# Performance work log

Hardware: AMD Instinct MI355X
Metric: run time of the kernel (lower is better)

Reference implementation:

```python
import jax, jax.numpy as jnp
import numpy as np

EPS = 1e-6
B, N, E = 2, 100000, 400000
NODE_DIM, NUM_FEAT = 32, 32
H0, H1 = 128, 64   # state_encoder_hidden_size
D = 64             # gcn_node_dim


def setup_inputs() -> dict:
    key = jax.random.key(0)
    ks = jax.random.split(key, 12)
    def lin(k, fan_in, shape):
        b = 1.0 / np.sqrt(fan_in)
        return jax.random.uniform(k, shape, jnp.float32, -b, b)
    return {
        "numerical": jax.random.normal(ks[0], (B, NUM_FEAT), jnp.float32),
        "node_feature": jax.random.normal(ks[1], (B, N, NODE_DIM), jnp.float32),
        "edge_index": jax.random.randint(ks[2], (B, E, 2), 0, N),
        "edge_mask": jax.random.randint(ks[3], (B, E), 0, 2).astype(bool),
        "stage": jax.random.normal(ks[4], (B, 2), jnp.float32),
        # numerical feature encoder: Linear(32->128) tanh, Linear(128->64) tanh
        "W1": lin(ks[5], NUM_FEAT, (NUM_FEAT, H0)), "b1": lin(ks[6], NUM_FEAT, (H0,)),
        "W2": lin(ks[7], H0, (H0, H1)), "b2": lin(ks[8], H0, (H1,)),
        # node encoder: Linear(32->64) tanh
        "Wn": lin(ks[9], NODE_DIM, (NODE_DIM, D)), "bn": lin(ks[10], NODE_DIM, (D,)),
        # edge_fc: Linear(128->64) tanh
        "We": lin(ks[11], 2 * D, (2 * D, D)),
        "be": lin(jax.random.fold_in(key, 99), 2 * D, (D,)),
    }


def reference(numerical, node_feature, edge_index, edge_mask, stage,
              W1, b1, W2, b2, Wn, bn, We, be):
    # numerical feature encoder
    h_num = jnp.tanh(jnp.tanh(numerical @ W1 + b1) @ W2 + b2)       # [B, H1]
    # node encoder
    h_nodes = jnp.tanh(node_feature @ Wn + bn)                       # [B, N, D]
    # gather node feats to edge endpoints
    h1 = jnp.take_along_axis(h_nodes, edge_index[:, :, 0:1], axis=1)  # [B, E, D]
    h2 = jnp.take_along_axis(h_nodes, edge_index[:, :, 1:2], axis=1)  # [B, E, D]
    # edge_fc applied to [h1,h2] and [h2,h1], averaged. Split We to avoid concat.
    Wa, Wb = We[:D], We[D:]
    e12 = jnp.tanh(h1 @ Wa + h2 @ Wb + be)
    e21 = jnp.tanh(h2 @ Wa + h1 @ Wb + be)
    h_edges = 0.5 * (e12 + e21)                                       # [B, E, D]
    m = edge_mask[:, :, None]
    h_edges = jnp.where(m, h_edges, 0.0)
    # masked mean over edges
    mf = edge_mask.astype(h_edges.dtype)
    h_mean = (h_edges * mf[:, :, None]).sum(axis=1) / mf.sum(axis=1, keepdims=True)
    state_value = jnp.concatenate([h_num, h_mean, stage], axis=-1)    # [B, H1+D+2]
    state_policy = h_edges                                            # [B, E, D]
    return (state_policy, state_value)
```

## Files before the change

### kernel.cpp

```cpp
#include <hip/hip_runtime.h>
#include <hip/hip_bf16.h>

typedef __attribute__((ext_vector_type(4))) float  f32x4;
typedef __attribute__((ext_vector_type(8))) __bf16 bf16x8;

#define NB 2
#define NN 100000
#define NE 400000
#define EPB 256

__device__ __forceinline__ float tanh_f(float x) {
  float y = __builtin_amdgcn_fmed3f(2.f * x, -40.f, 40.f);
  float e = __expf(y);
  return fmaf(-2.f, __builtin_amdgcn_rcpf(e + 1.f), 1.f);
}

__device__ __forceinline__ float ldf(const void* p, long i, int bf) {
  return bf ? (float)((const __bf16*)p)[i] : ((const float*)p)[i];
}

__global__ __launch_bounds__(256) void k_setup(
    const unsigned int* __restrict__ mw, const unsigned int* __restrict__ nodew,
    const void* __restrict__ numerical, const void* __restrict__ W1,
    const void* __restrict__ b1, const void* __restrict__ W2,
    const void* __restrict__ b2, const void* __restrict__ Wn,
    const void* __restrict__ bn, const void* __restrict__ We,
    int* __restrict__ flags, float* __restrict__ hnum,
    float* __restrict__ sums, float* __restrict__ counts,
    __bf16* __restrict__ packWn, __bf16* __restrict__ packWe,
    float* __restrict__ packBn) {
  __shared__ int badS, goodS, dtS;
  __shared__ float numf[2][32];
  __shared__ float u[2][128];
  const int t = threadIdx.x;
  if (t == 0) { badS = 0; goodS = 0; }
  __syncthreads();
  int my = 0;
  for (int i = t; i < 4096; i += 256) my |= (mw[i] > 1u) ? 1 : 0;
  if (my) atomicOr(&badS, 1);
  int g = 0;
  for (int i = t; i < 4096; i += 256) {
    unsigned lo = nodew[i] & 0xFFFFu;
    unsigned e = (lo >> 7) & 0xFFu;
    g += (lo == 0u || (e >= 100u && e <= 141u)) ? 1 : 0;
  }
  atomicAdd(&goodS, g);
  __syncthreads();
  if (t == 0) {
    flags[0] = badS;
    dtS = (goodS > 2048) ? 1 : 0;
    flags[1] = dtS;
  }
  __syncthreads();
  const int dt = dtS;

  if (t < 128) sums[t] = 0.f;
  if (t < 2) counts[t] = 0.f;
  if (t < 64) numf[t >> 5][t & 31] = ldf(numerical, t, dt);
  __syncthreads();
  {
    const int b = t >> 7, j = t & 127;
    float acc = ldf(b1, j, dt);
#pragma unroll
    for (int k = 0; k < 32; ++k) acc += numf[b][k] * ldf(W1, k * 128 + j, dt);
    u[b][j] = tanh_f(acc);
  }
  __syncthreads();
  if (t < 128) {
    const int b = t >> 6, d = t & 63;
    float acc = ldf(b2, d, dt);
#pragma unroll
    for (int k = 0; k < 128; ++k) acc += u[b][k] * ldf(W2, k * 64 + d, dt);
    hnum[b * 64 + d] = tanh_f(acc);
  }

  if (t < 64) {
    const int m = t & 15, quad = t >> 4;
#pragma unroll
    for (int nt = 0; nt < 4; ++nt) {
      const int c = m + 16 * nt;
#pragma unroll
      for (int j = 0; j < 8; ++j)
        packWn[t * 32 + nt * 8 + j] = (__bf16)ldf(Wn, (quad * 8 + j) * 64 + c, dt);
      packBn[t * 4 + nt] = ldf(bn, c, dt);
    }
#pragma unroll
    for (int f = 0; f < 16; ++f) {
      const int s = f >> 2, nt = f & 3;
      const int n = m + 16 * nt;
#pragma unroll
      for (int j = 0; j < 8; ++j) {
        const int k = s * 32 + quad * 8 + j;
        packWe[(f * 64 + t) * 8 + j] = (__bf16)ldf(We, (long)k * 64 + n, dt);
      }
    }
  }
}

__global__ __launch_bounds__(256) void k_nodes(
    const void* __restrict__ node, const __bf16* __restrict__ packWn,
    const float* __restrict__ packBn, const int* __restrict__ flags,
    __bf16* __restrict__ hG) {
  const int t = threadIdx.x;
  const int wave = t >> 6, lane = t & 63;
  const int m = lane & 15, quad = lane >> 4;
  const int dt = flags[1];

  bf16x8 wnF[4];
#pragma unroll
  for (int nt = 0; nt < 4; ++nt)
    wnF[nt] = *(const bf16x8*)(packWn + lane * 32 + nt * 8);
  float bnv[4];
#pragma unroll
  for (int nt = 0; nt < 4; ++nt) bnv[nt] = packBn[lane * 4 + nt];

  const long r0 = ((long)blockIdx.x * 4 + wave) * 16;
  bf16x8 aF;
  if (dt) {
    aF = *(const bf16x8*)((const __bf16*)node + (r0 + m) * 32 + quad * 8);
  } else {
    const float* p = (const float*)node + (r0 + m) * 32 + quad * 8;
    f32x4 v0 = *(const f32x4*)p, v1 = *(const f32x4*)(p + 4);
#pragma unroll
    for (int j = 0; j < 4; ++j) { aF[j] = (__bf16)v0[j]; aF[4 + j] = (__bf16)v1[j]; }
  }

  f32x4 acc[4];
#pragma unroll
  for (int nt = 0; nt < 4; ++nt) {
    f32x4 c; c[0] = bnv[nt]; c[1] = bnv[nt]; c[2] = bnv[nt]; c[3] = bnv[nt];
    acc[nt] = c;
  }
#pragma unroll
  for (int nt = 0; nt < 4; ++nt)
    acc[nt] = __builtin_amdgcn_mfma_f32_16x16x32_bf16(aF, wnF[nt], acc[nt], 0, 0, 0);

  __bf16* out = hG + r0 * 64;
#pragma unroll
  for (int nt = 0; nt < 4; ++nt)
#pragma unroll
    for (int r = 0; r < 4; ++r)
      out[(quad * 4 + r) * 64 + m + 16 * nt] = (__bf16)tanh_f(acc[nt][r]);
}

__global__ __launch_bounds__(256) void k_edges(
    const int2* __restrict__ eidx, const void* __restrict__ emask,
    const int* __restrict__ flags, const __bf16* __restrict__ hG,
    const __bf16* __restrict__ packWe, const void* __restrict__ be,
    float* __restrict__ sums, float* __restrict__ counts,
    float* __restrict__ outp) {
  const int nbPerB = (NE + EPB - 1) / EPB;
  const int b = blockIdx.x / nbPerB;
  const long e0 = (long)(blockIdx.x % nbPerB) * EPB;
  const int t = threadIdx.x;
  const int wave = t >> 6, lane = t & 63;
  const int m = lane & 15, quad = lane >> 4;
  const int dt = flags[1], mode = flags[0];

  __shared__ __bf16 weL[64 * 128];
  __shared__ int2 eL[EPB];
  __shared__ float mL[EPB];
  __shared__ float red[4][64];
  __shared__ float redc[4];

  {
    const bf16x8* src = (const bf16x8*)packWe;
    bf16x8* dst = (bf16x8*)weL;
#pragma unroll
    for (int u = 0; u < 4; ++u) dst[t + 256 * u] = src[t + 256 * u];
  }
  {
    const long e = e0 + t;
    const int valid = (e < NE) ? 1 : 0;
    const long ec = valid ? e : (NE - 1);
    eL[t] = eidx[(long)b * NE + ec];
    float mv;
    if (mode) mv = (float)(((const unsigned char*)emask)[(long)b * NE + ec]);
    else      mv = (float)(((const int*)emask)[(long)b * NE + ec]);
    mL[t] = valid ? mv : 0.f;
  }
  __syncthreads();

  float be2[4];
#pragma unroll
  for (int nt = 0; nt < 4; ++nt) be2[nt] = 2.f * ldf(be, m + 16 * nt, dt);

  const __bf16* hb = hG + (long)b * NN * 64;
  float psum[4] = {0.f, 0.f, 0.f, 0.f};

  bf16x8 a0, a1, a2, a3;
  {
    const int2 ij = eL[wave * 64 + m];
    const __bf16* hi = hb + (long)ij.x * 64;
    const __bf16* hj = hb + (long)ij.y * 64;
    a0 = *(const bf16x8*)(hi + quad * 8);
    a1 = *(const bf16x8*)(hi + 32 + quad * 8);
    a2 = *(const bf16x8*)(hj + quad * 8);
    a3 = *(const bf16x8*)(hj + 32 + quad * 8);
  }

#pragma unroll
  for (int it = 0; it < 4; ++it) {
    const int slot = wave * 64 + it * 16;
    const bf16x8 c0 = a0, c1 = a1, c2 = a2, c3 = a3;
    if (it < 3) {
      const int2 ij = eL[slot + 16 + m];
      const __bf16* hi = hb + (long)ij.x * 64;
      const __bf16* hj = hb + (long)ij.y * 64;
      a0 = *(const bf16x8*)(hi + quad * 8);
      a1 = *(const bf16x8*)(hi + 32 + quad * 8);
      a2 = *(const bf16x8*)(hj + quad * 8);
      a3 = *(const bf16x8*)(hj + 32 + quad * 8);
    }

    f32x4 acc12[4], acc21[4];
#pragma unroll
    for (int nt = 0; nt < 4; ++nt) {
      f32x4 z; z[0] = 0.f; z[1] = 0.f; z[2] = 0.f; z[3] = 0.f;
      acc12[nt] = z; acc21[nt] = z;
    }
#pragma unroll
    for (int s = 0; s < 4; ++s) {
      bf16x8 w[4];
#pragma unroll
      for (int nt = 0; nt < 4; ++nt)
        w[nt] = *(const bf16x8*)(weL + ((4 * s + nt) * 64 + lane) * 8);
      const bf16x8 a12 = (s == 0) ? c0 : (s == 1) ? c1 : (s == 2) ? c2 : c3;
      const bf16x8 a21 = (s == 0) ? c2 : (s == 1) ? c3 : (s == 2) ? c0 : c1;
#pragma unroll
      for (int nt = 0; nt < 4; ++nt) {
        acc12[nt] = __builtin_amdgcn_mfma_f32_16x16x32_bf16(a12, w[nt], acc12[nt], 0, 0, 0);
        acc21[nt] = __builtin_amdgcn_mfma_f32_16x16x32_bf16(a21, w[nt], acc21[nt], 0, 0, 0);
      }
    }

    const long egbase = e0 + slot;
#pragma unroll
    for (int r = 0; r < 4; ++r) {
      const long e = egbase + quad * 4 + r;
      if (e >= NE) continue;
      const float mvr = mL[slot + quad * 4 + r];
      float* op = outp + ((long)b * NE + e) * 64 + m;
#pragma unroll
      for (int nt = 0; nt < 4; ++nt) {
        float x12 = __builtin_amdgcn_fmed3f(
            fmaf(acc12[nt][r], 2.f, be2[nt]), -40.f, 40.f);
        float x21 = __builtin_amdgcn_fmed3f(
            fmaf(acc21[nt][r], 2.f, be2[nt]), -40.f, 40.f);
        const float p12 = __builtin_amdgcn_rcpf(__expf(x12) + 1.f);
        const float p21 = __builtin_amdgcn_rcpf(__expf(x21) + 1.f);
        const float v = mvr * (1.f - p12 - p21);
        psum[nt] += v;
        __builtin_nontemporal_store(v, op + 16 * nt);
      }
    }
  }

#pragma unroll
  for (int nt = 0; nt < 4; ++nt) {
    psum[nt] += __shfl_xor(psum[nt], 16);
    psum[nt] += __shfl_xor(psum[nt], 32);
  }
  if (quad == 0) {
#pragma unroll
    for (int nt = 0; nt < 4; ++nt) red[wave][m + 16 * nt] = psum[nt];
  }
  float pc = mL[t];
#pragma unroll
  for (int d = 1; d < 64; d <<= 1) pc += __shfl_xor(pc, d);
  if (lane == 0) redc[wave] = pc;
  __syncthreads();
  if (t < 64) {
    const float s = red[0][t] + red[1][t] + red[2][t] + red[3][t];
    atomicAdd(&sums[b * 64 + t], s);
  }
  if (t == 0) atomicAdd(&counts[b], redc[0] + redc[1] + redc[2] + redc[3]);
}

__global__ __launch_bounds__(512) void k_final(
    const float* __restrict__ hnum, const float* __restrict__ sums,
    const float* __restrict__ counts, const void* __restrict__ stage,
    const int* __restrict__ flags, float* __restrict__ out) {
  const int t = threadIdx.x;
  const int dt = flags[1];
  if (t < 260) {
    const int b = t / 130, c = t % 130;
    float v;
    if (c < 64) v = hnum[b * 64 + c];
    else if (c < 128) v = sums[b * 64 + (c - 64)] / counts[b];
    else v = ldf(stage, b * 2 + (c - 128), dt);
    out[(long)NB * NE * 64 + (long)b * 130 + c] = v;
  }
}

extern "C" void kernel_launch(void* const* d_in, const int* in_sizes, int n_in,
                              void* d_out, int out_size, void* d_ws, size_t ws_size,
                              hipStream_t stream) {
  const void* numerical = d_in[0];
  const void* node      = d_in[1];
  const int2* eidx      = (const int2*)d_in[2];
  const void* emask     = d_in[3];
  const void* stage     = d_in[4];
  const void* W1 = d_in[5];
  const void* b1 = d_in[6];
  const void* W2 = d_in[7];
  const void* b2 = d_in[8];
  const void* Wn = d_in[9];
  const void* bn = d_in[10];
  const void* We = d_in[11];
  const void* be = d_in[12];

  char* ws = (char*)d_ws;
  int*    flags  = (int*)ws;
  float*  sums   = (float*)(ws + 256);
  float*  counts = (float*)(ws + 1024);
  float*  hnum   = (float*)(ws + 1280);
  float*  packBn = (float*)(ws + 2048);
  __bf16* packWn = (__bf16*)(ws + 4096);
  __bf16* packWe = (__bf16*)(ws + 8192);
  __bf16* hG     = (__bf16*)(ws + 32768);
  float*  outp   = (float*)d_out;

  k_setup<<<1, 256, 0, stream>>>((const unsigned int*)emask, (const unsigned int*)node,
                                 numerical, W1, b1, W2, b2, Wn, bn, We,
                                 flags, hnum, sums, counts, packWn, packWe, packBn);
  k_nodes<<<(NB * NN) / 64, 256, 0, stream>>>(node, packWn, packBn, flags, hG);
  k_edges<<<NB * ((NE + EPB - 1) / EPB), 256, 0, stream>>>(eidx, emask, flags, hG, packWe, be,
                                                           sums, counts, outp);
  k_final<<<1, 512, 0, stream>>>(hnum, sums, counts, stage, flags, outp);
}
```

Baseline: 392.4 us.

## Compact masked-in edges per block and skip gather/MFMA for masked edges

Each block now uses a wave ballot and prefix count to build a compacted list of edges whose mask is set. It writes zeros directly for masked-out edges and runs the node gather, MFMA and tanh only on the kept edges, spread across waves in 16-edge tiles. This removes the gather bandwidth and compute spent on the roughly half of edges that are masked out, at the cost of an extra barrier, shared-memory index indirection and less regular store addresses. The two tanh calls are merged algebraically so one reciprocal replaces two, and the weight-packing setup is spread over all 256 threads.

```diff
diff --git a/kernel.cpp b/kernel.cpp
--- a/kernel.cpp
+++ b/kernel.cpp
@@ -84,14 +84,18 @@
         packWn[t * 32 + nt * 8 + j] = (__bf16)ldf(Wn, (quad * 8 + j) * 64 + c, dt);
       packBn[t * 4 + nt] = ldf(bn, c, dt);
     }
-#pragma unroll
-    for (int f = 0; f < 16; ++f) {
-      const int s = f >> 2, nt = f & 3;
-      const int n = m + 16 * nt;
+  }
+  {
+    const int lane = t & 63, fg = t >> 6;
+    const int m2 = lane & 15, quad2 = lane >> 4;
+#pragma unroll
+    for (int ff = 0; ff < 4; ++ff) {
+      const int f = fg * 4 + ff;
+      const int n = m2 + 16 * ff;
 #pragma unroll
       for (int j = 0; j < 8; ++j) {
-        const int k = s * 32 + quad * 8 + j;
-        packWe[(f * 64 + t) * 8 + j] = (__bf16)ldf(We, (long)k * 64 + n, dt);
+        const int k = fg * 32 + quad2 * 8 + j;
+        packWe[(f * 64 + lane) * 8 + j] = (__bf16)ldf(We, (long)k * 64 + n, dt);
       }
     }
   }
@@ -160,8 +164,9 @@
   __shared__ __bf16 weL[64 * 128];
   __shared__ int2 eL[EPB];
   __shared__ float mL[EPB];
+  __shared__ unsigned short cS[EPB];
+  __shared__ int wcnt[4];
   __shared__ float red[4][64];
-  __shared__ float redc[4];
 
   {
     const bf16x8* src = (const bf16x8*)packWe;
@@ -169,6 +174,7 @@
 #pragma unroll
     for (int u = 0; u < 4; ++u) dst[t + 256 * u] = src[t + 256 * u];
   }
+  int kept;
   {
     const long e = e0 + t;
     const int valid = (e < NE) ? 1 : 0;
@@ -177,41 +183,69 @@
     float mv;
     if (mode) mv = (float)(((const unsigned char*)emask)[(long)b * NE + ec]);
     else      mv = (float)(((const int*)emask)[(long)b * NE + ec]);
-    mL[t] = valid ? mv : 0.f;
-  }
-  __syncthreads();
+    mv = valid ? mv : 0.f;
+    mL[t] = mv;
+    kept = (mv != 0.f) ? 1 : 0;
+  }
+  const unsigned long long bal = __ballot(kept);
+  const int lpos = __popcll(bal & ((1ull << lane) - 1ull));
+  if (lane == 0) wcnt[wave] = __popcll(bal);
+  __syncthreads();
+
+  int woff = 0, cntTot = 0;
+#pragma unroll
+  for (int w = 0; w < 4; ++w) {
+    cntTot += wcnt[w];
+    if (w < wave) woff += wcnt[w];
+  }
+  if (kept) cS[woff + lpos] = (unsigned short)t;
+
+  {
+    const int g = lane >> 2, gi = lane & 3;
+    const f32x4 z = {0.f, 0.f, 0.f, 0.f};
+#pragma unroll
+    for (int p = 0; p < 4; ++p) {
+      const int slot = wave * 64 + p * 16 + g;
+      const long e = e0 + slot;
+      if (e < NE && mL[slot] == 0.f) {
+        float* op = outp + ((long)b * NE + e) * 64 + gi * 16;
+        __builtin_nontemporal_store(z, (f32x4*)op);
+        __builtin_nontemporal_store(z, (f32x4*)(op + 4));
+        __builtin_nontemporal_store(z, (f32x4*)(op + 8));
+        __builtin_nontemporal_store(z, (f32x4*)(op + 12));
+      }
+    }
+  }
 
   float be2[4];
 #pragma unroll
   for (int nt = 0; nt < 4; ++nt) be2[nt] = 2.f * ldf(be, m + 16 * nt, dt);
+  __syncthreads();
 
   const __bf16* hb = hG + (long)b * NN * 64;
+  const int ntiles = (cntTot + 15) >> 4;
   float psum[4] = {0.f, 0.f, 0.f, 0.f};
 
   bf16x8 a0, a1, a2, a3;
-  {
-    const int2 ij = eL[wave * 64 + m];
-    const __bf16* hi = hb + (long)ij.x * 64;
-    const __bf16* hj = hb + (long)ij.y * 64;
-    a0 = *(const bf16x8*)(hi + quad * 8);
-    a1 = *(const bf16x8*)(hi + 32 + quad * 8);
-    a2 = *(const bf16x8*)(hj + quad * 8);
-    a3 = *(const bf16x8*)(hj + 32 + quad * 8);
-  }
-
-#pragma unroll
-  for (int it = 0; it < 4; ++it) {
-    const int slot = wave * 64 + it * 16;
+#define GATHERT(TB)                                                 \
+  {                                                                 \
+    int idx_ = (TB) + m;                                            \
+    if (idx_ >= cntTot) idx_ = cntTot - 1;                          \
+    const int s_ = cS[idx_];                                        \
+    const int2 ij = eL[s_];                                         \
+    const __bf16* hi = hb + (long)ij.x * 64;                        \
+    const __bf16* hj = hb + (long)ij.y * 64;                        \
+    a0 = *(const bf16x8*)(hi + quad * 8);                           \
+    a1 = *(const bf16x8*)(hi + 32 + quad * 8);                      \
+    a2 = *(const bf16x8*)(hj + quad * 8);                           \
+    a3 = *(const bf16x8*)(hj + 32 + quad * 8);                      \
+  }
+
+  int tt = wave;
+  if (tt < ntiles) GATHERT(tt * 16)
+  for (; tt < ntiles; tt += 4) {
     const bf16x8 c0 = a0, c1 = a1, c2 = a2, c3 = a3;
-    if (it < 3) {
-      const int2 ij = eL[slot + 16 + m];
-      const __bf16* hi = hb + (long)ij.x * 64;
-      const __bf16* hj = hb + (long)ij.y * 64;
-      a0 = *(const bf16x8*)(hi + quad * 8);
-      a1 = *(const bf16x8*)(hi + 32 + quad * 8);
-      a2 = *(const bf16x8*)(hj + quad * 8);
-      a3 = *(const bf16x8*)(hj + 32 + quad * 8);
-    }
+    if (tt + 4 < ntiles) GATHERT((tt + 4) * 16)
 
     f32x4 acc12[4], acc21[4];
 #pragma unroll
@@ -234,27 +268,29 @@
       }
     }
 
-    const long egbase = e0 + slot;
 #pragma unroll
     for (int r = 0; r < 4; ++r) {
-      const long e = egbase + quad * 4 + r;
-      if (e >= NE) continue;
-      const float mvr = mL[slot + quad * 4 + r];
+      const int erow = tt * 16 + quad * 4 + r;
+      if (erow >= cntTot) continue;
+      const long e = e0 + cS[erow];
       float* op = outp + ((long)b * NE + e) * 64 + m;
 #pragma unroll
       for (int nt = 0; nt < 4; ++nt) {
-        float x12 = __builtin_amdgcn_fmed3f(
+        const float x12 = __builtin_amdgcn_fmed3f(
             fmaf(acc12[nt][r], 2.f, be2[nt]), -40.f, 40.f);
-        float x21 = __builtin_amdgcn_fmed3f(
+        const float x21 = __builtin_amdgcn_fmed3f(
             fmaf(acc21[nt][r], 2.f, be2[nt]), -40.f, 40.f);
-        const float p12 = __builtin_amdgcn_rcpf(__expf(x12) + 1.f);
-        const float p21 = __builtin_amdgcn_rcpf(__expf(x21) + 1.f);
-        const float v = mvr * (1.f - p12 - p21);
+        const float E1 = __expf(x12);
+        const float E2 = __expf(x21);
+        const float sE = E1 + E2;
+        const float den = fmaf(E1, E2, sE + 1.f);
+        const float v = fmaf(-(sE + 2.f), __builtin_amdgcn_rcpf(den), 1.f);
         psum[nt] += v;
         __builtin_nontemporal_store(v, op + 16 * nt);
       }
     }
   }
+#undef GATHERT
 
 #pragma unroll
   for (int nt = 0; nt < 4; ++nt) {
@@ -265,16 +301,12 @@
 #pragma unroll
     for (int nt = 0; nt < 4; ++nt) red[wave][m + 16 * nt] = psum[nt];
   }
-  float pc = mL[t];
-#pragma unroll
-  for (int d = 1; d < 64; d <<= 1) pc += __shfl_xor(pc, d);
-  if (lane == 0) redc[wave] = pc;
   __syncthreads();
   if (t < 64) {
     const float s = red[0][t] + red[1][t] + red[2][t] + red[3][t];
     atomicAdd(&sums[b * 64 + t], s);
   }
-  if (t == 0) atomicAdd(&counts[b], redc[0] + redc[1] + redc[2] + redc[3]);
+  if (t == 0) atomicAdd(&counts[b], (float)cntTot);
 }
 
 __global__ __launch_bounds__(512) void k_final(
```

Result: faster. 354.9 us (median of 2 runs) (-9.5%).
